# Optimization experiments

Measured on AMD Instinct MI355X. Metric: run time of the kernel, lower is better.

Reference implementation:

```python
import jax, jax.numpy as jnp
import numpy as np

B, C, H, W = 16, 512, 64, 64


def setup_inputs() -> dict:
    key = jax.random.key(0)
    ks = jax.random.split(key, 8)
    s = 1.0 / np.sqrt(C)  # fan-in scale like torch conv default
    return {
        "x": jax.random.normal(ks[0], (B, C, H, W), dtype=jnp.float32),
        "y": jax.random.normal(ks[1], (B, C), dtype=jnp.float32),
        "wq": jax.random.normal(ks[2], (C, C), dtype=jnp.float32) * s,
        "bq": jax.random.normal(ks[3], (C,), dtype=jnp.float32) * s,
        "wk": jax.random.normal(ks[4], (C, C), dtype=jnp.float32) * s,
        "bk": jax.random.normal(ks[5], (C,), dtype=jnp.float32) * s,
        "wv": jax.random.normal(ks[6], (C, C), dtype=jnp.float32) * s,
        "bv": jax.random.normal(ks[7], (C,), dtype=jnp.float32) * s,
        "gamma": jnp.ones((1,), dtype=jnp.float32),
    }


def _conv1x1_flat(inp_flat, w, b):
    # inp_flat: (B, C, N); 1x1 conv == per-pixel channel GEMM
    return jnp.einsum("oc,bcn->bon", w, inp_flat) + b[None, :, None]


def reference(x, y, wq, bq, wk, bk, wv, bv, gamma):
    b, c, h, w = x.shape
    n = h * w
    # align=True: y (B, C) broadcast to (B, C, H, W); flatten spatial dims
    y_flat = jnp.broadcast_to(y[:, :, None], (b, c, n))
    x_flat = x.reshape(b, c, n)
    # exchange=False: q = y, k = v = x
    pq = _conv1x1_flat(y_flat, wq, bq)          # (B, C, N)
    pk = _conv1x1_flat(x_flat, wk, bk)          # (B, C, N)
    pv = _conv1x1_flat(x_flat, wv, bv)          # (B, C, N)
    energy = jnp.einsum("bcn,bdn->bcd", pq, pk)  # (B, C, C) channel attention
    attn = jax.nn.softmax(energy, axis=-1)
    out = jnp.einsum("bcd,bdn->bcn", attn, pv)   # (B, C, N)
    out = out.reshape(b, c, h, w)
    return gamma * out + x
```

## Files before the change

### kernel.cpp

```cpp
#include <hip/hip_runtime.h>
#include <hip/hip_bf16.h>

#define Bn 16
#define Cn 512
#define Nn 4096

typedef unsigned short u16;
typedef __bf16 bf16x8 __attribute__((ext_vector_type(8)));
typedef float f32x4 __attribute__((ext_vector_type(4)));
typedef unsigned short u16x8 __attribute__((ext_vector_type(8)));

__device__ __forceinline__ u16 f2bf(float f) {
    __hip_bfloat16 h = __float2bfloat16(f);
    return *reinterpret_cast<u16*>(&h);
}

__device__ __forceinline__ void glds16(const u16* g, u16* l) {
    __builtin_amdgcn_global_load_lds(
        (const __attribute__((address_space(1))) void*)g,
        (__attribute__((address_space(3))) void*)l, 16, 0, 0);
}

__global__ __launch_bounds__(256) void k_transpose(
    const float* __restrict__ x, u16* __restrict__ xt, float* __restrict__ sxp)
{
    __shared__ float tile[128 * 65];
    const int b = blockIdx.z, c0 = blockIdx.y * 128, n0 = blockIdx.x * 64;
    const int t = threadIdx.x;
    const float* xb = x + ((size_t)(b * Cn + c0)) * Nn + n0;

    float part[8];
#pragma unroll
    for (int r = 0; r < 8; ++r) {
        int cl = (t >> 4) + r * 16;
        int nl = (t & 15) * 4;
        float4 v = *(const float4*)(xb + (size_t)cl * Nn + nl);
        float* tp = &tile[cl * 65 + nl];
        tp[0] = v.x; tp[1] = v.y; tp[2] = v.z; tp[3] = v.w;
        part[r] = (v.x + v.y) + (v.z + v.w);
    }
#pragma unroll
    for (int m = 1; m < 16; m <<= 1) {
#pragma unroll
        for (int r = 0; r < 8; ++r) part[r] += __shfl_xor(part[r], m);
    }
    if ((t & 15) == 0) {
#pragma unroll
        for (int r = 0; r < 8; ++r) {
            int cl = (t >> 4) + r * 16;
            sxp[(size_t)(b * Cn + c0 + cl) * 64 + blockIdx.x] = part[r];
        }
    }
    __syncthreads();
    u16* xtb = xt + ((size_t)(b * Nn + n0)) * Cn + c0;
#pragma unroll
    for (int r = 0; r < 4; ++r) {
        int nl = (t >> 4) + r * 16;
        int c8 = (t & 15) * 8;
        u16x8 hv;
#pragma unroll
        for (int i = 0; i < 8; ++i) hv[i] = f2bf(tile[(c8 + i) * 65 + nl]);
        *(u16x8*)(xtb + (size_t)nl * Cn + c8) = hv;
    }
}

__global__ __launch_bounds__(256) void k_sxred(
    const float* __restrict__ sxp, float* __restrict__ sx)
{
    int i = blockIdx.x * 256 + threadIdx.x;
    const float4* p = (const float4*)(sxp + (size_t)i * 64);
    float s = 0.f;
#pragma unroll
    for (int j = 0; j < 16; ++j) {
        float4 v = p[j];
        s += (v.x + v.y) + (v.z + v.w);
    }
    sx[i] = s;
}

__global__ __launch_bounds__(256) void k_qk(
    const float* __restrict__ wq, const float* __restrict__ bq,
    const float* __restrict__ wk, const float* __restrict__ bk,
    const float* __restrict__ y, const float* __restrict__ sx,
    float* __restrict__ qy, float* __restrict__ sk)
{
    const int w = threadIdx.x >> 6, lane = threadIdx.x & 63;
    const int o = blockIdx.x * 4 + w;
    const int b = blockIdx.y;
    const int mode = blockIdx.z;
    const float* W = mode ? wk : wq;
    const float* vec = mode ? (sx + b * Cn) : (y + b * Cn);
    float sum = 0.f;
#pragma unroll
    for (int i = 0; i < 8; ++i) {
        int k2 = lane + i * 64;
        sum += W[(size_t)o * Cn + k2] * vec[k2];
    }
#pragma unroll
    for (int m = 1; m < 64; m <<= 1) sum += __shfl_xor(sum, m);
    if (lane == 0) {
        if (mode) sk[b * Cn + o] = sum + 4096.0f * bk[o];
        else      qy[b * Cn + o] = sum + bq[o];
    }
}

__global__ __launch_bounds__(256) void k_wvt(
    const float* __restrict__ wv, u16* __restrict__ wvt)
{
    __shared__ float tl[64 * 65];
    const int d0 = blockIdx.x * 64, e0 = blockIdx.y * 64;
    const int t = threadIdx.x;
#pragma unroll
    for (int r = 0; r < 4; ++r) {
        int d = (t >> 4) + r * 16, e4 = (t & 15) * 4;
        float4 v = *(const float4*)(wv + (size_t)(d0 + d) * Cn + e0 + e4);
        float* p = &tl[d * 65 + e4];
        p[0] = v.x; p[1] = v.y; p[2] = v.z; p[3] = v.w;
    }
    __syncthreads();
#pragma unroll
    for (int r = 0; r < 4; ++r) {
        int e = (t >> 4) + r * 16, d4 = (t & 15) * 4;
        ushort4 h;
        h.x = f2bf(tl[(d4 + 0) * 65 + e]);
        h.y = f2bf(tl[(d4 + 1) * 65 + e]);
        h.z = f2bf(tl[(d4 + 2) * 65 + e]);
        h.w = f2bf(tl[(d4 + 3) * 65 + e]);
        *(ushort4*)(wvt + (size_t)(e0 + e) * Cn + d0 + d4) = h;
    }
}

__global__ __launch_bounds__(256) void k_softmax(
    const float* __restrict__ qy, const float* __restrict__ sk,
    const float* __restrict__ bv, u16* __restrict__ attn,
    float* __restrict__ beff, const float* __restrict__ gamma)
{
    __shared__ float red[4], red2[4], red3[4];
    const int b = blockIdx.x >> 9, c = blockIdx.x & 511;
    const int t = threadIdx.x;
    const float q = qy[b * Cn + c];
    const float l0 = q * sk[b * Cn + t];
    const float l1 = q * sk[b * Cn + t + 256];
    float mx = fmaxf(l0, l1);
#pragma unroll
    for (int m = 1; m < 64; m <<= 1) mx = fmaxf(mx, __shfl_xor(mx, m));
    if ((t & 63) == 0) red[t >> 6] = mx;
    __syncthreads();
    mx = fmaxf(fmaxf(red[0], red[1]), fmaxf(red[2], red[3]));
    const float e0 = __expf(l0 - mx), e1 = __expf(l1 - mx);
    float s = e0 + e1;
#pragma unroll
    for (int m = 1; m < 64; m <<= 1) s += __shfl_xor(s, m);
    if ((t & 63) == 0) red2[t >> 6] = s;
    __syncthreads();
    s = red2[0] + red2[1] + red2[2] + red2[3];
    const float inv = 1.0f / s;
    const float a0 = e0 * inv, a1 = e1 * inv;
    u16* arow = attn + ((size_t)(b * Cn + c)) * Cn;
    arow[t] = f2bf(a0);
    arow[t + 256] = f2bf(a1);
    float pb = a0 * bv[t] + a1 * bv[t + 256];
#pragma unroll
    for (int m = 1; m < 64; m <<= 1) pb += __shfl_xor(pb, m);
    if ((t & 63) == 0) red3[t >> 6] = pb;
    __syncthreads();
    if (t == 0)
        beff[b * Cn + c] = gamma[0] * (red3[0] + red3[1] + red3[2] + red3[3]);
}

template <int FINAL>
__global__ __launch_bounds__(256) void k_gemm(
    const u16* __restrict__ A, size_t strideA,
    const u16* __restrict__ Bt, size_t strideB,
    int N,
    u16* __restrict__ outBf, size_t strideOb,
    float* __restrict__ outF,
    const float* __restrict__ xres,
    const float* __restrict__ beff,
    const float* __restrict__ gamma)
{
    constexpr int K = 512;
    __shared__ float smem_f[8448];
    u16* la = (u16*)smem_f;
    u16* lb = la + 128 * 64;
    const int b = blockIdx.z;
    const int m0 = blockIdx.y * 128;
    const int n0 = blockIdx.x * 128;
    A  += (size_t)b * strideA;
    Bt += (size_t)b * strideB;
    const int t = threadIdx.x;
    const int lane = t & 63;
    const int w = t >> 6;
    const int wm = (w >> 1) * 64, wn = (w & 1) * 64;
    const int l15 = lane & 15, quad = lane >> 4;

    f32x4 acc[4][4];
#pragma unroll
    for (int i = 0; i < 4; ++i)
#pragma unroll
        for (int j = 0; j < 4; ++j)
            acc[i][j] = (f32x4){0.f, 0.f, 0.f, 0.f};

    const int srow8 = lane >> 3;
    const int lgcol = ((lane & 7) ^ srow8) * 8;

    for (int k0 = 0; k0 < K; k0 += 64) {
        __syncthreads();
#pragma unroll
        for (int j = 0; j < 4; ++j) {
            const int row = w * 32 + j * 8 + srow8;
            const int sb = (w * 256 + j * 64) * 8;
            glds16(A  + (size_t)(m0 + row) * K + k0 + lgcol, la + sb);
            glds16(Bt + (size_t)(n0 + row) * K + k0 + lgcol, lb + sb);
        }
        __syncthreads();

#pragma unroll
        for (int kk2 = 0; kk2 < 2; ++kk2) {
            bf16x8 af[4], bfr[4];
#pragma unroll
            for (int mi = 0; mi < 4; ++mi) {
                const int r = wm + mi * 16 + l15;
                const int pg = ((kk2 << 2) + quad) ^ (l15 & 7);
                af[mi] = *(const bf16x8*)&la[r * 64 + pg * 8];
            }
#pragma unroll
            for (int ni = 0; ni < 4; ++ni) {
                const int r = wn + ni * 16 + l15;
                const int pg = ((kk2 << 2) + quad) ^ (l15 & 7);
                bfr[ni] = *(const bf16x8*)&lb[r * 64 + pg * 8];
            }
#pragma unroll
            for (int mi = 0; mi < 4; ++mi)
#pragma unroll
                for (int ni = 0; ni < 4; ++ni)
                    acc[mi][ni] = __builtin_amdgcn_mfma_f32_16x16x32_bf16(
                        af[mi], bfr[ni], acc[mi][ni], 0, 0, 0);
        }
    }

    if (FINAL) {
        float* lc = smem_f;
#pragma unroll
        for (int h = 0; h < 2; ++h) {
            __syncthreads();
            if ((w >> 1) == h) {
#pragma unroll
                for (int mi = 0; mi < 4; ++mi)
#pragma unroll
                    for (int reg = 0; reg < 4; ++reg) {
                        const int rl = mi * 16 + quad * 4 + reg;
#pragma unroll
                        for (int ni = 0; ni < 4; ++ni)
                            lc[rl * 132 + wn + ni * 16 + l15] = acc[mi][ni][reg];
                    }
            }
            __syncthreads();
            const int rb = h * 64;
#pragma unroll
            for (int rr = 0; rr < 8; ++rr) {
                const int rl = rr * 8 + (t >> 5);
                const int c4 = (t & 31) * 4;
                float4 v = *(float4*)&lc[rl * 132 + c4];
                const int r = m0 + rb + rl;
                const float be = beff[b * Cn + r];
                const size_t base = ((size_t)(b * Cn + r)) * N + n0 + c4;
                float4 xr = *(const float4*)(xres + base);
                float4 o;
                o.x = (v.x + be) + xr.x;
                o.y = (v.y + be) + xr.y;
                o.z = (v.z + be) + xr.z;
                o.w = (v.w + be) + xr.w;
                *(float4*)(outF + base) = o;
            }
        }
    } else {
        const float gs = gamma[0];
#pragma unroll
        for (int mi = 0; mi < 4; ++mi) {
#pragma unroll
            for (int reg = 0; reg < 4; ++reg) {
                const int r = m0 + wm + mi * 16 + quad * 4 + reg;
                const size_t base = (size_t)b * strideOb + (size_t)r * N;
#pragma unroll
                for (int ni = 0; ni < 4; ++ni) {
                    const int cidx = n0 + wn + ni * 16 + l15;
                    outBf[base + cidx] = f2bf(gs * acc[mi][ni][reg]);
                }
            }
        }
    }
}

__global__ __launch_bounds__(512, 4) void k_gemm2(
    const u16* __restrict__ A,
    const u16* __restrict__ Bt,
    float* __restrict__ outF,
    const float* __restrict__ xres,
    const float* __restrict__ beff)
{
    extern __shared__ u16 sm[];
    const int b = blockIdx.z;
    const int m0 = blockIdx.y << 8;
    const int n0 = blockIdx.x << 7;
    const int t = threadIdx.x;
    const int lane = t & 63, w = t >> 6;
    const int wm = (w >> 1) << 6, wn = (w & 1) << 6;
    const int l15 = lane & 15, quad = lane >> 4;

    const u16* Ag = A + (size_t)b * Cn * Cn;
    const u16* Bg = Bt + (size_t)b * ((size_t)Nn * Cn);
    const int srow = t >> 2;
    const int scol = (((t & 3) ^ ((srow >> 1) & 3))) << 3;
    const u16* pa = Ag + (size_t)(m0 + srow) * Cn + scol;
    const u16* pb = Bg + (size_t)(n0 + srow) * Cn + scol;
    const int dwo = w * 512;

#define STGA(s, c, k0) \
    glds16(pa + (size_t)(c) * (128 * Cn) + (k0), \
           sm + (s) * 8192 + (c) * 4096 + dwo)
#define STGB(s, k0) glds16(pb + (k0), sm + 24576 + (s) * 4096 + dwo)
#define FRGA(s, row, qd) \
    (*(const bf16x8*)&sm[(s) * 8192 + (row) * 32 + \
                         (((qd) ^ (((row) >> 1) & 3)) << 3)])
#define FRGB(s, row, qd) \
    (*(const bf16x8*)&sm[24576 + (s) * 4096 + (row) * 32 + \
                         (((qd) ^ (((row) >> 1) & 3)) << 3)])

    f32x4 acc[4][4];
#pragma unroll
    for (int mi = 0; mi < 4; ++mi)
#pragma unroll
        for (int reg = 0; reg < 4; ++reg) {
            const int row = m0 + wm + mi * 16 + quad * 4 + reg;
            const float* xr =
                xres + ((size_t)(b * Cn + row)) * Nn + n0 + wn + l15;
#pragma unroll
            for (int ni = 0; ni < 4; ++ni)
                acc[mi][ni][reg] = xr[ni * 16];
        }
    asm volatile("" ::: "memory");
    __builtin_amdgcn_sched_barrier(0);

    STGB(0, 0);
    STGA(0, 0, 0); STGA(0, 1, 0);
    STGB(1, 32);
    STGA(1, 0, 32); STGA(1, 1, 32);
    STGB(2, 64);

#pragma unroll
    for (int tI = 0; tI < 16; ++tI) {
        if (tI <= 13)      { asm volatile("s_waitcnt vmcnt(4)" ::: "memory"); }
        else if (tI == 14) { asm volatile("s_waitcnt vmcnt(3)" ::: "memory"); }
        else               { asm volatile("s_waitcnt vmcnt(0)" ::: "memory"); }
        __builtin_amdgcn_s_barrier();
        if (tI + 2 <= 15) {
            STGA((tI + 2) % 3, 0, (tI + 2) << 5);
            STGA((tI + 2) % 3, 1, (tI + 2) << 5);
        }
        if (tI + 3 <= 15) {
            STGB((tI + 3) & 3, (tI + 3) << 5);
        }
        const int sa = tI % 3, sb4 = tI & 3;
        bf16x8 af[4], bf[4];
#pragma unroll
        for (int mi = 0; mi < 4; ++mi)
            af[mi] = FRGA(sa, wm + mi * 16 + l15, quad);
#pragma unroll
        for (int ni = 0; ni < 4; ++ni)
            bf[ni] = FRGB(sb4, wn + ni * 16 + l15, quad);
        __builtin_amdgcn_s_setprio(1);
#pragma unroll
        for (int mi = 0; mi < 4; ++mi)
#pragma unroll
            for (int ni = 0; ni < 4; ++ni)
                acc[mi][ni] = __builtin_amdgcn_mfma_f32_16x16x32_bf16(
                    af[mi], bf[ni], acc[mi][ni], 0, 0, 0);
        __builtin_amdgcn_s_setprio(0);
    }
#undef STGA
#undef STGB
#undef FRGA
#undef FRGB

    __syncthreads();
    float* lc = (float*)sm;
#pragma unroll
    for (int h = 0; h < 4; ++h) {
        if (h) __syncthreads();
        if ((w >> 1) == h) {
#pragma unroll
            for (int mi = 0; mi < 4; ++mi)
#pragma unroll
                for (int reg = 0; reg < 4; ++reg) {
                    const int rl = mi * 16 + quad * 4 + reg;
#pragma unroll
                    for (int ni = 0; ni < 4; ++ni)
                        lc[rl * 132 + wn + ni * 16 + l15] = acc[mi][ni][reg];
                }
        }
        __syncthreads();
#pragma unroll
        for (int k = 0; k < 4; ++k) {
            const int r = (t >> 5) + k * 16;
            const int c4 = (t & 31) * 4;
            f32x4 v = *(f32x4*)&lc[r * 132 + c4];
            const int row = m0 + h * 64 + r;
            const float be = beff[b * Cn + row];
            const size_t base = ((size_t)(b * Cn + row)) * Nn + n0 + c4;
            f32x4 o;
            o[0] = v[0] + be;
            o[1] = v[1] + be;
            o[2] = v[2] + be;
            o[3] = v[3] + be;
            __builtin_nontemporal_store(o, (f32x4*)(outF + base));
        }
    }
}

extern "C" void kernel_launch(void* const* d_in, const int* in_sizes, int n_in,
                              void* d_out, int out_size, void* d_ws, size_t ws_size,
                              hipStream_t stream)
{
    const float* x     = (const float*)d_in[0];
    const float* y     = (const float*)d_in[1];
    const float* wq    = (const float*)d_in[2];
    const float* bq    = (const float*)d_in[3];
    const float* wk    = (const float*)d_in[4];
    const float* bk    = (const float*)d_in[5];
    const float* wv    = (const float*)d_in[6];
    const float* bv    = (const float*)d_in[7];
    const float* gamma = (const float*)d_in[8];
    float* out = (float*)d_out;

    char* ws = (char*)d_ws;
    u16*   xt   = (u16*)  (ws + 0);
    float* sxp  = (float*)(ws + 67108864);
    float* sx   = (float*)(ws + 69206016);
    float* qy   = (float*)(ws + 69238784);
    float* sk   = (float*)(ws + 69271552);
    float* beff = (float*)(ws + 69304320);
    u16*   attn = (u16*)  (ws + 69337088);
    u16*   wvt  = (u16*)  (ws + 77725696);
    u16*   weff = (u16*)  (ws + 78249984);

    k_transpose<<<dim3(64, 4, Bn), dim3(256), 0, stream>>>(x, xt, sxp);
    k_sxred<<<dim3(32), dim3(256), 0, stream>>>(sxp, sx);
    k_wvt<<<dim3(8, 8), dim3(256), 0, stream>>>(wv, wvt);
    k_qk<<<dim3(128, Bn, 2), dim3(256), 0, stream>>>(wq, bq, wk, bk, y, sx, qy, sk);
    k_softmax<<<dim3(Bn * Cn), dim3(256), 0, stream>>>(qy, sk, bv, attn, beff, gamma);
    k_gemm<0><<<dim3(4, 4, Bn), dim3(256), 0, stream>>>(
        attn, (size_t)Cn * Cn, wvt, (size_t)0, Cn,
        weff, (size_t)Cn * Cn, nullptr, nullptr, nullptr, gamma);
    if (hipFuncSetAttribute((const void*)k_gemm2,
                            hipFuncAttributeMaxDynamicSharedMemorySize,
                            81920) == hipSuccess) {
        k_gemm2<<<dim3(32, 2, Bn), dim3(512), 81920, stream>>>(
            weff, xt, out, x, beff);
    } else {
        k_gemm<1><<<dim3(32, 4, Bn), dim3(256), 0, stream>>>(
            weff, (size_t)Cn * Cn, xt, (size_t)Nn * Cn, Nn,
            nullptr, (size_t)0, out, x, beff, gamma);
    }
}
```

Before: 331.6 us.

## Fuse rank-1 softmax into Weff GEMM, generating attention on the fly

```diff
diff --git a/kernel.cpp b/kernel.cpp
--- a/kernel.cpp
+++ b/kernel.cpp
@@ -130,42 +130,138 @@
     }
 }
 
-__global__ __launch_bounds__(256) void k_softmax(
+__global__ __launch_bounds__(256) void k_weff(
     const float* __restrict__ qy, const float* __restrict__ sk,
-    const float* __restrict__ bv, u16* __restrict__ attn,
-    float* __restrict__ beff, const float* __restrict__ gamma)
-{
-    __shared__ float red[4], red2[4], red3[4];
-    const int b = blockIdx.x >> 9, c = blockIdx.x & 511;
+    const float* __restrict__ bv, const u16* __restrict__ wvt,
+    u16* __restrict__ weff, float* __restrict__ beff,
+    const float* __restrict__ gamma)
+{
+    __shared__ u16 lb[128 * 64];
+    __shared__ float sk_l[512], bv_l[512], qy_l[128], mx_l[128], id_l[128];
+    __shared__ float red[8];
+    const int b = blockIdx.z, m0 = blockIdx.y * 128, n0 = blockIdx.x * 128;
     const int t = threadIdx.x;
-    const float q = qy[b * Cn + c];
-    const float l0 = q * sk[b * Cn + t];
-    const float l1 = q * sk[b * Cn + t + 256];
-    float mx = fmaxf(l0, l1);
-#pragma unroll
-    for (int m = 1; m < 64; m <<= 1) mx = fmaxf(mx, __shfl_xor(mx, m));
-    if ((t & 63) == 0) red[t >> 6] = mx;
+    const int lane = t & 63, w = t >> 6;
+    const int wm = (w >> 1) * 64, wn = (w & 1) * 64;
+    const int l15 = lane & 15, quad = lane >> 4;
+    const float gs = gamma[0];
+
+    sk_l[t] = sk[b * Cn + t];
+    sk_l[t + 256] = sk[b * Cn + t + 256];
+    bv_l[t] = bv[t];
+    bv_l[t + 256] = bv[t + 256];
+    if (t < 128) qy_l[t] = qy[b * Cn + m0 + t];
     __syncthreads();
-    mx = fmaxf(fmaxf(red[0], red[1]), fmaxf(red[2], red[3]));
-    const float e0 = __expf(l0 - mx), e1 = __expf(l1 - mx);
-    float s = e0 + e1;
-#pragma unroll
-    for (int m = 1; m < 64; m <<= 1) s += __shfl_xor(s, m);
-    if ((t & 63) == 0) red2[t >> 6] = s;
+
+    {
+        float a = sk_l[t], c2 = sk_l[t + 256];
+        float smx = fmaxf(a, c2), smn = fminf(a, c2);
+#pragma unroll
+        for (int m = 1; m < 64; m <<= 1) {
+            smx = fmaxf(smx, __shfl_xor(smx, m));
+            smn = fminf(smn, __shfl_xor(smn, m));
+        }
+        if (lane == 0) { red[w] = smx; red[4 + w] = smn; }
+    }
     __syncthreads();
-    s = red2[0] + red2[1] + red2[2] + red2[3];
-    const float inv = 1.0f / s;
-    const float a0 = e0 * inv, a1 = e1 * inv;
-    u16* arow = attn + ((size_t)(b * Cn + c)) * Cn;
-    arow[t] = f2bf(a0);
-    arow[t + 256] = f2bf(a1);
-    float pb = a0 * bv[t] + a1 * bv[t + 256];
-#pragma unroll
-    for (int m = 1; m < 64; m <<= 1) pb += __shfl_xor(pb, m);
-    if ((t & 63) == 0) red3[t >> 6] = pb;
+    const float skmax = fmaxf(fmaxf(red[0], red[1]), fmaxf(red[2], red[3]));
+    const float skmin = fminf(fminf(red[4], red[5]), fminf(red[6], red[7]));
+
+    {
+        const int r = t >> 1, hf = t & 1;
+        const float q = qy_l[r];
+        const float mxr = (q >= 0.f) ? q * skmax : q * skmin;
+        float den = 0.f, bac = 0.f;
+        const int dbase = hf * 256;
+#pragma unroll 8
+        for (int j = 0; j < 256; ++j) {
+            const float e = __expf(q * sk_l[dbase + j] - mxr);
+            den += e;
+            bac += e * bv_l[dbase + j];
+        }
+        den += __shfl_xor(den, 1);
+        bac += __shfl_xor(bac, 1);
+        if (hf == 0) {
+            mx_l[r] = mxr;
+            const float inv = 1.0f / den;
+            id_l[r] = inv;
+            if (blockIdx.x == 0) beff[b * Cn + m0 + r] = gs * bac * inv;
+        }
+    }
     __syncthreads();
-    if (t == 0)
-        beff[b * Cn + c] = gamma[0] * (red3[0] + red3[1] + red3[2] + red3[3]);
+
+    float qv[4], mxv[4], idv[4];
+#pragma unroll
+    for (int mi = 0; mi < 4; ++mi) {
+        const int row = wm + mi * 16 + l15;
+        qv[mi] = qy_l[row];
+        mxv[mi] = mx_l[row];
+        idv[mi] = id_l[row];
+    }
+
+    f32x4 acc[4][4];
+#pragma unroll
+    for (int i = 0; i < 4; ++i)
+#pragma unroll
+        for (int j = 0; j < 4; ++j)
+            acc[i][j] = (f32x4){0.f, 0.f, 0.f, 0.f};
+
+    const int srow8 = lane >> 3;
+    const int lgcol = ((lane & 7) ^ srow8) * 8;
+
+    for (int k0 = 0; k0 < 512; k0 += 64) {
+        __syncthreads();
+#pragma unroll
+        for (int j = 0; j < 4; ++j) {
+            const int row = w * 32 + j * 8 + srow8;
+            const int sb = (w * 256 + j * 64) * 8;
+            glds16(wvt + (size_t)(n0 + row) * Cn + k0 + lgcol, lb + sb);
+        }
+        __syncthreads();
+
+#pragma unroll
+        for (int kk2 = 0; kk2 < 2; ++kk2) {
+            const int d0 = k0 + ((kk2 << 2) + quad) * 8;
+            f32x4 s0 = *(const f32x4*)&sk_l[d0];
+            f32x4 s1 = *(const f32x4*)&sk_l[d0 + 4];
+            bf16x8 af[4], bfr[4];
+#pragma unroll
+            for (int mi = 0; mi < 4; ++mi) {
+                const float q = qv[mi], mo = mxv[mi], iv = idv[mi];
+#pragma unroll
+                for (int j = 0; j < 4; ++j) {
+                    af[mi][j] = (__bf16)(__expf(q * s0[j] - mo) * iv);
+                    af[mi][j + 4] = (__bf16)(__expf(q * s1[j] - mo) * iv);
+                }
+            }
+#pragma unroll
+            for (int ni = 0; ni < 4; ++ni) {
+                const int r = wn + ni * 16 + l15;
+                const int pg = ((kk2 << 2) + quad) ^ (l15 & 7);
+                bfr[ni] = *(const bf16x8*)&lb[r * 64 + pg * 8];
+            }
+#pragma unroll
+            for (int mi = 0; mi < 4; ++mi)
+#pragma unroll
+                for (int ni = 0; ni < 4; ++ni)
+                    acc[mi][ni] = __builtin_amdgcn_mfma_f32_16x16x32_bf16(
+                        af[mi], bfr[ni], acc[mi][ni], 0, 0, 0);
+        }
+    }
+
+#pragma unroll
+    for (int mi = 0; mi < 4; ++mi) {
+#pragma unroll
+        for (int reg = 0; reg < 4; ++reg) {
+            const int r = m0 + wm + mi * 16 + quad * 4 + reg;
+            const size_t base = (size_t)b * (Cn * Cn) + (size_t)r * Cn;
+#pragma unroll
+            for (int ni = 0; ni < 4; ++ni) {
+                const int cidx = n0 + wn + ni * 16 + l15;
+                weff[base + cidx] = f2bf(gs * acc[mi][ni][reg]);
+            }
+        }
+    }
 }
 
 template <int FINAL>
@@ -440,7 +536,6 @@
     float* qy   = (float*)(ws + 69238784);
     float* sk   = (float*)(ws + 69271552);
     float* beff = (float*)(ws + 69304320);
-    u16*   attn = (u16*)  (ws + 69337088);
     u16*   wvt  = (u16*)  (ws + 77725696);
     u16*   weff = (u16*)  (ws + 78249984);
 
@@ -448,10 +543,8 @@
     k_sxred<<<dim3(32), dim3(256), 0, stream>>>(sxp, sx);
     k_wvt<<<dim3(8, 8), dim3(256), 0, stream>>>(wv, wvt);
     k_qk<<<dim3(128, Bn, 2), dim3(256), 0, stream>>>(wq, bq, wk, bk, y, sx, qy, sk);
-    k_softmax<<<dim3(Bn * Cn), dim3(256), 0, stream>>>(qy, sk, bv, attn, beff, gamma);
-    k_gemm<0><<<dim3(4, 4, Bn), dim3(256), 0, stream>>>(
-        attn, (size_t)Cn * Cn, wvt, (size_t)0, Cn,
-        weff, (size_t)Cn * Cn, nullptr, nullptr, nullptr, gamma);
+    k_weff<<<dim3(4, 4, Bn), dim3(256), 0, stream>>>(
+        qy, sk, bv, wvt, weff, beff, gamma);
     if (hipFuncSetAttribute((const void*)k_gemm2,
                             hipFuncAttributeMaxDynamicSharedMemorySize,
                             81920) == hipSuccess) {
```

After: 329.0 us. Within noise of the previous version (-0.8%).
